# Kernel optimization log

Hardware: AMD Instinct MI355X
Metric: run time of the kernel (lower is better)

The kernel has to match this reference:

```python
import jax, jax.numpy as jnp
import numpy as np

WINDOW = 12
NUM_HEADS = 16

def window_partition(x, ws):
    b, h, w, c = x.shape
    x = x.reshape(b, h // ws, ws, w // ws, ws, c)
    return x.transpose(0, 1, 3, 2, 4, 5).reshape(-1, ws, ws, c)

def window_reverse(windows, ws, h, w):
    c = windows.shape[-1]
    x = windows.reshape(-1, h // ws, w // ws, ws, ws, c)
    return x.transpose(0, 1, 3, 2, 4, 5).reshape(-1, h, w, c)

def setup_inputs() -> dict:
    key = jax.random.key(0)
    ks = jax.random.split(key, 5)
    dim = 512
    hidden_states = jax.random.normal(ks[0], (8, 48, 48, dim), dtype=jnp.float32)
    qkv_w = jax.random.normal(ks[1], (dim, 3 * dim), dtype=jnp.float32) * 0.02
    qkv_b = jnp.zeros((3 * dim,), dtype=jnp.float32)
    proj_w = jax.random.normal(ks[2], (dim, dim), dtype=jnp.float32) * 0.02
    proj_b = jnp.zeros((dim,), dtype=jnp.float32)
    return {"hidden_states": hidden_states, "qkv_w": qkv_w, "qkv_b": qkv_b,
            "proj_w": proj_w, "proj_b": proj_b}

def reference(hidden_states, qkv_w, qkv_b, proj_w, proj_b):
    b, h, w, c = hidden_states.shape
    ws = WINDOW
    nh = NUM_HEADS
    hd = c // nh
    scale = hd ** -0.5
    pad_r = (ws - w % ws) % ws
    pad_b = (ws - h % ws) % ws
    x = jnp.pad(hidden_states, ((0, 0), (0, pad_b), (0, pad_r), (0, 0)))
    ph, pw = x.shape[1], x.shape[2]
    # [nW, ws*ws, C]
    xw = window_partition(x, ws).reshape(-1, ws * ws, c)
    nw, nt, _ = xw.shape
    qkv = (xw @ qkv_w + qkv_b).reshape(nw, nt, 3, nh, hd)
    qkv = qkv.transpose(2, 0, 3, 1, 4)  # [3, nW, nh, nt, hd]
    q, k, v = qkv[0], qkv[1], qkv[2]
    scores = jnp.einsum('wnqd,wnkd->wnqk', q, k) * scale
    attn = jax.nn.softmax(scores, axis=-1)
    out = jnp.einsum('wnqk,wnkd->wnqd', attn, v)  # [nW, nh, nt, hd]
    out = out.transpose(0, 2, 1, 3).reshape(nw, nt, c)
    out = out @ proj_w + proj_b
    out = out.reshape(-1, ws, ws, c)
    out = window_reverse(out, ws, ph, pw)
    out = out[:, :h, :w, :]
    return out.reshape(b, h * w, c)
```

## Files before the change

kernel.cpp:

```cpp
#include <hip/hip_runtime.h>
#include <hip/hip_bf16.h>


typedef unsigned short u16;
typedef unsigned int u32;
typedef __attribute__((ext_vector_type(4))) float f32x4;
typedef __attribute__((ext_vector_type(8))) short short8;

#define MFMA16(a, b, c) __builtin_amdgcn_mfma_f32_16x16x32_bf16(a, b, c, 0, 0, 0)
#define AS1 __attribute__((address_space(1)))
#define AS3 __attribute__((address_space(3)))

__device__ __forceinline__ u16 f2b(float f) {
  __hip_bfloat16 h = __float2bfloat16(f);
  return *reinterpret_cast<u16*>(&h);
}

__global__ void prep_x_kernel(const float* __restrict__ x, u16* __restrict__ xw) {
  int c = blockIdx.x * 256 + threadIdx.x;
  int r = c >> 6;
  int colb = (c & 63) << 3;
  int win = r / 144, tok = r - win * 144;
  int b = win >> 4, wh = (win >> 2) & 3, ww = win & 3;
  int i = tok / 12, j = tok - i * 12;
  const float* src = x + ((size_t)((b * 48 + wh * 12 + i) * 48 + ww * 12 + j)) * 512 + colb;
  float4 a0 = *(const float4*)(src);
  float4 a1 = *(const float4*)(src + 4);
  short8 o;
  o[0] = (short)f2b(a0.x); o[1] = (short)f2b(a0.y); o[2] = (short)f2b(a0.z); o[3] = (short)f2b(a0.w);
  o[4] = (short)f2b(a1.x); o[5] = (short)f2b(a1.y); o[6] = (short)f2b(a1.z); o[7] = (short)f2b(a1.w);
  *reinterpret_cast<short8*>(xw + (size_t)r * 512 + colb) = o;
}

__global__ void prep_wt_kernel(const float* __restrict__ w, u16* __restrict__ wt,
                               int K, int N) {
  int t = blockIdx.x * 256 + threadIdx.x;
  int nchunks = N >> 3;
  if (t >= K * nchunks) return;
  int k = t / nchunks;
  int n0 = (t - k * nchunks) << 3;
  const float* src = w + (size_t)k * N + n0;
  float4 a0 = *(const float4*)(src);
  float4 a1 = *(const float4*)(src + 4);
  float v[8] = {a0.x, a0.y, a0.z, a0.w, a1.x, a1.y, a1.z, a1.w};
#pragma unroll
  for (int j = 0; j < 8; j++) wt[(size_t)(n0 + j) * K + k] = f2b(v[j]);
}

template <int BM, int BN, int WM, int WN, int EPI>
__device__ __forceinline__ void gemm_impl(
    const u16* __restrict__ A, const u16* __restrict__ BT,
    const float* __restrict__ bias,
    u16* __restrict__ outb, float* __restrict__ outf,
    int M, int N, int K) {
  constexpr int MF = BM / WM / 16;
  constexpr int NF = BN / WN / 16;
  constexpr int ASLOT = BM * 32;
  constexpr int BSLOT = BN * 32;
  __shared__ __align__(16) u16 sA[4 * ASLOT];
  __shared__ __align__(16) u16 sB[4 * BSLOT];

  const int tid = threadIdx.x;
  const int wave = tid >> 6;
  const int lane = tid & 63;
  const int wm = wave / WN;
  const int wn = wave % WN;
  const int l15 = lane & 15;
  const int lhi = lane >> 4;

  const int nwg = gridDim.x;
  const int cpx = nwg >> 3;
  const int bid = (blockIdx.x & 7) * cpx + (blockIdx.x >> 3);
  const int nbn = N / BN;
  const int bn = bid % nbn;
  const int bm = bid / nbn;

  f32x4 acc[MF][NF];
  const f32x4 fzero = {0.f, 0.f, 0.f, 0.f};
#pragma unroll
  for (int i = 0; i < MF; i++)
#pragma unroll
    for (int j = 0; j < NF; j++) acc[i][j] = fzero;

  const int srow = lane >> 2;
  const int scol = (((lane & 3) ^ ((lane >> 3) & 3)) << 3);
  const int rcol = ((lhi ^ ((l15 >> 1) & 3)) << 3);

  const u16* Ab = A + (size_t)(bm * BM) * K;
  const u16* Bb = BT + (size_t)(bn * BN) * K;
  const int nt = K >> 5;

  auto stage = [&](int l, int tt) {
    const int slot = tt & 3;
    const int kk = tt << 5;
    if (l < 2) {
      const int c = wave * 2 + l;
      __builtin_amdgcn_global_load_lds(
          (const AS1 u32*)(Ab + (size_t)(c * 16 + srow) * K + kk + scol),
          (AS3 u32*)(&sA[slot * ASLOT + c * 512]), 16, 0, 0);
    } else {
      const int c = wave * 2 + (l - 2);
      __builtin_amdgcn_global_load_lds(
          (const AS1 u32*)(Bb + (size_t)(c * 16 + srow) * K + kk + scol),
          (AS3 u32*)(&sB[slot * BSLOT + c * 512]), 16, 0, 0);
    }
  };

#pragma unroll
  for (int t0 = 0; t0 < 3; ++t0)
#pragma unroll
    for (int l = 0; l < 4; ++l) stage(l, t0);

  for (int t = 0; t < nt; ++t) {
    const int cur = t & 3;
    const bool has3 = (t + 3 < nt);
    const int rem = nt - 1 - t;

    if (rem >= 2)      { asm volatile("s_waitcnt vmcnt(8)"); }
    else if (rem == 1) { asm volatile("s_waitcnt vmcnt(4)"); }
    else               { asm volatile("s_waitcnt vmcnt(0)"); }
    __builtin_amdgcn_sched_barrier(0);
    __builtin_amdgcn_s_barrier();
    __builtin_amdgcn_sched_barrier(0);

    const u16* pA = &sA[cur * ASLOT];
    const u16* pB = &sB[cur * BSLOT];

    short8 af[MF], bfr[NF];
#pragma unroll
    for (int m = 0; m < MF; ++m)
      af[m] = *reinterpret_cast<const short8*>(
          pA + (wm * (MF * 16) + m * 16 + l15) * 32 + rcol);
#pragma unroll
    for (int n = 0; n < NF; ++n)
      bfr[n] = *reinterpret_cast<const short8*>(
          pB + (wn * (NF * 16) + n * 16 + l15) * 32 + rcol);
    __builtin_amdgcn_sched_barrier(0);

    if (has3) {
#pragma unroll
      for (int l = 0; l < 4; ++l) stage(l, t + 3);
    }
    __builtin_amdgcn_sched_barrier(0);

    __builtin_amdgcn_s_setprio(1);
#pragma unroll
    for (int m = 0; m < MF; ++m)
#pragma unroll
      for (int n = 0; n < NF; ++n)
        acc[m][n] = MFMA16(af[m], bfr[n], acc[m][n]);
    __builtin_amdgcn_s_setprio(0);

    __builtin_amdgcn_sched_barrier(0);
    __builtin_amdgcn_s_barrier();
  }

#pragma unroll
  for (int i = 0; i < MF; ++i) {
    const int row0 = bm * BM + wm * (MF * 16) + i * 16 + lhi * 4;
#pragma unroll
    for (int j = 0; j < NF; ++j) {
      const int col = bn * BN + wn * (NF * 16) + j * 16 + l15;
      const float bv = bias[col];
#pragma unroll
      for (int r = 0; r < 4; ++r) {
        float v = acc[i][j][r] + bv;
        const int row = row0 + r;
        if (EPI == 0) {
          outb[(size_t)row * N + col] = f2b(v);
        } else {
          int win = row / 144, tok = row - win * 144;
          int b = win >> 4, wh = (win >> 2) & 3, ww = win & 3;
          int ii = tok / 12, jj = tok - ii * 12;
          size_t o = ((size_t)b * 2304 + (wh * 12 + ii) * 48 + (ww * 12 + jj)) * 512 + col;
          outf[o] = v;
        }
      }
    }
  }
}

__global__ __launch_bounds__(512, 1) void qkv_gemm(
    const u16* __restrict__ A, const u16* __restrict__ BT,
    const float* __restrict__ bias, u16* __restrict__ outb,
    int M, int N, int K) {
  gemm_impl<256, 256, 2, 4, 0>(A, BT, bias, outb, nullptr, M, N, K);
}

__global__ __launch_bounds__(256, 2) void proj_gemm(
    const u16* __restrict__ A, const u16* __restrict__ BT,
    const float* __restrict__ bias, float* __restrict__ outf,
    int M, int N, int K) {
  gemm_impl<128, 128, 2, 2, 1>(A, BT, bias, nullptr, outf, M, N, K);
}

__global__ __launch_bounds__(192) void attn_kernel(const u16* __restrict__ qkv,
                                                   u16* __restrict__ outb) {
  constexpr int PSTR = 168;
  __shared__ __align__(16) u16 sVT[32 * PSTR];
  __shared__ __align__(16) u16 sP[3 * 16 * PSTR];
  const int tid = threadIdx.x;
  const int wave = tid >> 6;
  const int lane = tid & 63;
  const int l15 = lane & 15;
  const int lhi = lane >> 4;
  const int win = blockIdx.x;
  const int head = blockIdx.y;
  const size_t base = ((size_t)win * 144) * 1536 + head * 32;
  const u16* Q = qkv + base;
  const u16* Kp = qkv + base + 512;
  const u16* V = qkv + base + 1024;
  constexpr float SC2 = 0.25509915922608635f;
  const f32x4 fzero = {0.f, 0.f, 0.f, 0.f};

  short8 vv[3];
  int vtok[3], vdb[3];
#pragma unroll
  for (int it = 0; it < 3; ++it) {
    int t = tid + it * 192;
    vtok[it] = t >> 2; vdb[it] = t & 3;
    vv[it] = *reinterpret_cast<const short8*>(V + (size_t)vtok[it] * 1536 + vdb[it] * 8);
  }
  short8 qa[3];
#pragma unroll
  for (int mt = 0; mt < 3; mt++) {
    int row = wave * 48 + mt * 16 + l15;
    qa[mt] = *reinterpret_cast<const short8*>(Q + (size_t)row * 1536 + lhi * 8);
  }
  short8 kb[9];
#pragma unroll
  for (int nt = 0; nt < 9; nt++) {
    int ctok = nt * 16 + l15;
    kb[nt] = *reinterpret_cast<const short8*>(Kp + (size_t)ctok * 1536 + lhi * 8);
  }

#pragma unroll
  for (int it = 0; it < 3; ++it) {
#pragma unroll
    for (int j = 0; j < 8; j++) sVT[(vdb[it] * 8 + j) * PSTR + vtok[it]] = (u16)vv[it][j];
  }
  for (int t = tid; t < 512; t += 192) {
    int d = t >> 4, cc = 144 + (t & 15);
    sVT[d * PSTR + cc] = 0;
  }
  u16* sPw = sP + wave * 16 * PSTR;
  for (int t = lane; t < 256; t += 64) {
    int rr = t >> 4, cc = 144 + (t & 15);
    sPw[rr * PSTR + cc] = 0;
  }

  __syncthreads();

  f32x4 o[3][2];
#pragma unroll
  for (int mt = 0; mt < 3; mt++)
#pragma unroll
    for (int nt = 0; nt < 2; nt++) o[mt][nt] = fzero;

#pragma unroll
  for (int mt = 0; mt < 3; mt++) {
    f32x4 s[9];
#pragma unroll
    for (int nt = 0; nt < 9; nt++) s[nt] = MFMA16(qa[mt], kb[nt], fzero);

#pragma unroll
    for (int r = 0; r < 4; r++) {
      float p[9], sum = 0.f;
#pragma unroll
      for (int nt = 0; nt < 9; nt++) {
        p[nt] = exp2f(s[nt][r] * SC2);
        sum += p[nt];
      }
#pragma unroll
      for (int off = 1; off < 16; off <<= 1) sum += __shfl_xor(sum, off, 64);
      float inv = 1.f / sum;
      int prow = lhi * 4 + r;
#pragma unroll
      for (int nt = 0; nt < 9; nt++)
        sPw[prow * PSTR + nt * 16 + l15] = f2b(p[nt] * inv);
    }

#pragma unroll
    for (int kk = 0; kk < 5; kk++) {
      short8 pa = *reinterpret_cast<const short8*>(sPw + l15 * PSTR + kk * 32 + lhi * 8);
#pragma unroll
      for (int nt = 0; nt < 2; nt++) {
        short8 vb = *reinterpret_cast<const short8*>(sVT + (nt * 16 + l15) * PSTR + kk * 32 + lhi * 8);
        o[mt][nt] = MFMA16(pa, vb, o[mt][nt]);
      }
    }
  }

  const int rowb = win * 144 + wave * 48;
#pragma unroll
  for (int mt = 0; mt < 3; mt++) {
#pragma unroll
    for (int nt = 0; nt < 2; nt++) {
      int col = head * 32 + nt * 16 + l15;
#pragma unroll
      for (int r = 0; r < 4; r++) {
        int row = rowb + mt * 16 + lhi * 4 + r;
        outb[(size_t)row * 512 + col] = f2b(o[mt][nt][r]);
      }
    }
  }
}

extern "C" void kernel_launch(void* const* d_in, const int* in_sizes, int n_in,
                              void* d_out, int out_size, void* d_ws, size_t ws_size,
                              hipStream_t stream) {
  const float* x      = (const float*)d_in[0];
  const float* qkv_w  = (const float*)d_in[1];
  const float* qkv_b  = (const float*)d_in[2];
  const float* proj_w = (const float*)d_in[3];
  const float* proj_b = (const float*)d_in[4];
  float* out = (float*)d_out;

  u16* xw     = (u16*)d_ws;
  u16* qkvT   = xw + (size_t)18432 * 512;
  u16* projT  = qkvT + (size_t)1536 * 512;
  u16* qkvout = projT + (size_t)512 * 512;
  u16* attno  = qkvout + (size_t)18432 * 1536;

  prep_x_kernel<<<4608, 256, 0, stream>>>(x, xw);
  prep_wt_kernel<<<384, 256, 0, stream>>>(qkv_w, qkvT, 512, 1536);
  prep_wt_kernel<<<128, 256, 0, stream>>>(proj_w, projT, 512, 512);

  qkv_gemm<<<432, 512, 0, stream>>>(xw, qkvT, qkv_b, qkvout, 18432, 1536, 512);

  attn_kernel<<<dim3(128, 16), 192, 0, stream>>>(qkvout, attno);

  proj_gemm<<<576, 256, 0, stream>>>(attno, projT, proj_b, out, 18432, 512, 512);
}
```

Measured before the change: 191.4 us.

## Write QKV in per-window-head layout with pre-transposed V; retile GEMMs

The QKV GEMM epilogue now scatters Q and K into contiguous per-(window,head) blocks and writes V already transposed with a padded stride. The attention kernel can then load V straight into LDS with global_load_lds, and its Q/K loads become contiguous. A new kernel clears the V padding columns. The GEMM pipeline drops from four LDS stages to two with a single barrier per step, and the QKV GEMM moves to 128x128 tiles with more blocks and higher occupancy. In exchange, the QKV epilogue stores become scattered 2-byte writes, and the shallower pipeline exposes more load latency.

```diff
diff --git a/kernel.cpp b/kernel.cpp
--- a/kernel.cpp
+++ b/kernel.cpp
@@ -10,6 +10,10 @@
 #define MFMA16(a, b, c) __builtin_amdgcn_mfma_f32_16x16x32_bf16(a, b, c, 0, 0, 0)
 #define AS1 __attribute__((address_space(1)))
 #define AS3 __attribute__((address_space(3)))
+
+constexpr size_t QTOT = (size_t)2048 * 4608;
+constexpr int VSTR = 176;
+constexpr size_t VWH = 32 * VSTR;
 
 __device__ __forceinline__ u16 f2b(float f) {
   __hip_bfloat16 h = __float2bfloat16(f);
@@ -47,6 +51,14 @@
   for (int j = 0; j < 8; j++) wt[(size_t)(n0 + j) * K + k] = f2b(v[j]);
 }
 
+__global__ void pad_clear_kernel(u16* __restrict__ vs) {
+  int wh = blockIdx.x;
+  int t = threadIdx.x;
+  int d = t >> 2, c = 144 + (t & 3) * 8;
+  short8 z = {0, 0, 0, 0, 0, 0, 0, 0};
+  *reinterpret_cast<short8*>(vs + (size_t)wh * VWH + d * VSTR + c) = z;
+}
+
 template <int BM, int BN, int WM, int WN, int EPI>
 __device__ __forceinline__ void gemm_impl(
     const u16* __restrict__ A, const u16* __restrict__ BT,
@@ -57,8 +69,8 @@
   constexpr int NF = BN / WN / 16;
   constexpr int ASLOT = BM * 32;
   constexpr int BSLOT = BN * 32;
-  __shared__ __align__(16) u16 sA[4 * ASLOT];
-  __shared__ __align__(16) u16 sB[4 * BSLOT];
+  __shared__ __align__(16) u16 sA[2 * ASLOT];
+  __shared__ __align__(16) u16 sB[2 * BSLOT];
 
   const int tid = threadIdx.x;
   const int wave = tid >> 6;
@@ -91,7 +103,7 @@
   const int nt = K >> 5;
 
   auto stage = [&](int l, int tt) {
-    const int slot = tt & 3;
+    const int slot = tt & 1;
     const int kk = tt << 5;
     if (l < 2) {
       const int c = wave * 2 + l;
@@ -107,18 +119,12 @@
   };
 
 #pragma unroll
-  for (int t0 = 0; t0 < 3; ++t0)
-#pragma unroll
-    for (int l = 0; l < 4; ++l) stage(l, t0);
+  for (int l = 0; l < 4; ++l) stage(l, 0);
 
   for (int t = 0; t < nt; ++t) {
-    const int cur = t & 3;
-    const bool has3 = (t + 3 < nt);
-    const int rem = nt - 1 - t;
-
-    if (rem >= 2)      { asm volatile("s_waitcnt vmcnt(8)"); }
-    else if (rem == 1) { asm volatile("s_waitcnt vmcnt(4)"); }
-    else               { asm volatile("s_waitcnt vmcnt(0)"); }
+    const int cur = t & 1;
+
+    asm volatile("s_waitcnt vmcnt(0)");
     __builtin_amdgcn_sched_barrier(0);
     __builtin_amdgcn_s_barrier();
     __builtin_amdgcn_sched_barrier(0);
@@ -137,9 +143,9 @@
           pB + (wn * (NF * 16) + n * 16 + l15) * 32 + rcol);
     __builtin_amdgcn_sched_barrier(0);
 
-    if (has3) {
-#pragma unroll
-      for (int l = 0; l < 4; ++l) stage(l, t + 3);
+    if (t + 1 < nt) {
+#pragma unroll
+      for (int l = 0; l < 4; ++l) stage(l, t + 1);
     }
     __builtin_amdgcn_sched_barrier(0);
 
@@ -150,9 +156,6 @@
       for (int n = 0; n < NF; ++n)
         acc[m][n] = MFMA16(af[m], bfr[n], acc[m][n]);
     __builtin_amdgcn_s_setprio(0);
-
-    __builtin_amdgcn_sched_barrier(0);
-    __builtin_amdgcn_s_barrier();
   }
 
 #pragma unroll
@@ -168,87 +171,94 @@
         const int row = row0 + r;
         if (EPI == 0) {
           outb[(size_t)row * N + col] = f2b(v);
-        } else {
+        } else if (EPI == 1) {
           int win = row / 144, tok = row - win * 144;
           int b = win >> 4, wh = (win >> 2) & 3, ww = win & 3;
           int ii = tok / 12, jj = tok - ii * 12;
           size_t o = ((size_t)b * 2304 + (wh * 12 + ii) * 48 + (ww * 12 + jj)) * 512 + col;
           outf[o] = v;
+        } else {
+          int dg = col & 511;
+          int typ = col >> 9;
+          int head = dg >> 5, d = dg & 31;
+          int win = row / 144, tok = row - win * 144;
+          int wh = win * 16 + head;
+          u16 bv16 = f2b(v);
+          if (typ == 0)
+            outb[(size_t)wh * 4608 + tok * 32 + d] = bv16;
+          else if (typ == 1)
+            outb[QTOT + (size_t)wh * 4608 + tok * 32 + d] = bv16;
+          else
+            outb[2 * QTOT + (size_t)wh * VWH + d * VSTR + tok] = bv16;
         }
       }
     }
   }
 }
 
-__global__ __launch_bounds__(512, 1) void qkv_gemm(
+__global__ __launch_bounds__(256, 4) void qkv_gemm(
     const u16* __restrict__ A, const u16* __restrict__ BT,
     const float* __restrict__ bias, u16* __restrict__ outb,
     int M, int N, int K) {
-  gemm_impl<256, 256, 2, 4, 0>(A, BT, bias, outb, nullptr, M, N, K);
-}
-
-__global__ __launch_bounds__(256, 2) void proj_gemm(
+  gemm_impl<128, 128, 2, 2, 2>(A, BT, bias, outb, nullptr, M, N, K);
+}
+
+__global__ __launch_bounds__(256, 4) void proj_gemm(
     const u16* __restrict__ A, const u16* __restrict__ BT,
     const float* __restrict__ bias, float* __restrict__ outf,
     int M, int N, int K) {
   gemm_impl<128, 128, 2, 2, 1>(A, BT, bias, nullptr, outf, M, N, K);
 }
 
-__global__ __launch_bounds__(192) void attn_kernel(const u16* __restrict__ qkv,
+__global__ __launch_bounds__(192) void attn_kernel(const u16* __restrict__ qkvs,
                                                    u16* __restrict__ outb) {
   constexpr int PSTR = 168;
-  __shared__ __align__(16) u16 sVT[32 * PSTR];
+  __shared__ __align__(16) u16 sVT[32 * VSTR];
   __shared__ __align__(16) u16 sP[3 * 16 * PSTR];
   const int tid = threadIdx.x;
   const int wave = tid >> 6;
   const int lane = tid & 63;
   const int l15 = lane & 15;
   const int lhi = lane >> 4;
-  const int win = blockIdx.x;
-  const int head = blockIdx.y;
-  const size_t base = ((size_t)win * 144) * 1536 + head * 32;
-  const u16* Q = qkv + base;
-  const u16* Kp = qkv + base + 512;
-  const u16* V = qkv + base + 1024;
+  const int wh = blockIdx.x;
+  const int win = wh >> 4;
+  const int head = wh & 15;
+  const u16* Q = qkvs + (size_t)wh * 4608;
+  const u16* Kp = qkvs + QTOT + (size_t)wh * 4608;
+  const u16* V = qkvs + 2 * QTOT + (size_t)wh * VWH;
   constexpr float SC2 = 0.25509915922608635f;
   const f32x4 fzero = {0.f, 0.f, 0.f, 0.f};
 
-  short8 vv[3];
-  int vtok[3], vdb[3];
-#pragma unroll
-  for (int it = 0; it < 3; ++it) {
-    int t = tid + it * 192;
-    vtok[it] = t >> 2; vdb[it] = t & 3;
-    vv[it] = *reinterpret_cast<const short8*>(V + (size_t)vtok[it] * 1536 + vdb[it] * 8);
-  }
+#pragma unroll
+  for (int i = 0; i < 4; ++i) {
+    const int c = wave * 4 + i;
+    if (c < 11) {
+      __builtin_amdgcn_global_load_lds(
+          (const AS1 u32*)(V + c * 512 + lane * 8),
+          (AS3 u32*)(&sVT[c * 512]), 16, 0, 0);
+    }
+  }
+
   short8 qa[3];
 #pragma unroll
   for (int mt = 0; mt < 3; mt++) {
     int row = wave * 48 + mt * 16 + l15;
-    qa[mt] = *reinterpret_cast<const short8*>(Q + (size_t)row * 1536 + lhi * 8);
+    qa[mt] = *reinterpret_cast<const short8*>(Q + row * 32 + lhi * 8);
   }
   short8 kb[9];
 #pragma unroll
   for (int nt = 0; nt < 9; nt++) {
     int ctok = nt * 16 + l15;
-    kb[nt] = *reinterpret_cast<const short8*>(Kp + (size_t)ctok * 1536 + lhi * 8);
-  }
-
-#pragma unroll
-  for (int it = 0; it < 3; ++it) {
-#pragma unroll
-    for (int j = 0; j < 8; j++) sVT[(vdb[it] * 8 + j) * PSTR + vtok[it]] = (u16)vv[it][j];
-  }
-  for (int t = tid; t < 512; t += 192) {
-    int d = t >> 4, cc = 144 + (t & 15);
-    sVT[d * PSTR + cc] = 0;
-  }
+    kb[nt] = *reinterpret_cast<const short8*>(Kp + ctok * 32 + lhi * 8);
+  }
+
   u16* sPw = sP + wave * 16 * PSTR;
   for (int t = lane; t < 256; t += 64) {
     int rr = t >> 4, cc = 144 + (t & 15);
     sPw[rr * PSTR + cc] = 0;
   }
 
+  asm volatile("s_waitcnt vmcnt(0)");
   __syncthreads();
 
   f32x4 o[3][2];
@@ -285,7 +295,7 @@
       short8 pa = *reinterpret_cast<const short8*>(sPw + l15 * PSTR + kk * 32 + lhi * 8);
 #pragma unroll
       for (int nt = 0; nt < 2; nt++) {
-        short8 vb = *reinterpret_cast<const short8*>(sVT + (nt * 16 + l15) * PSTR + kk * 32 + lhi * 8);
+        short8 vb = *reinterpret_cast<const short8*>(sVT + (nt * 16 + l15) * VSTR + kk * 32 + lhi * 8);
         o[mt][nt] = MFMA16(pa, vb, o[mt][nt]);
       }
     }
@@ -319,16 +329,17 @@
   u16* xw     = (u16*)d_ws;
   u16* qkvT   = xw + (size_t)18432 * 512;
   u16* projT  = qkvT + (size_t)1536 * 512;
-  u16* qkvout = projT + (size_t)512 * 512;
-  u16* attno  = qkvout + (size_t)18432 * 1536;
+  u16* qkvs   = projT + (size_t)512 * 512;
+  u16* attno  = qkvs + 2 * QTOT + (size_t)2048 * VWH;
 
   prep_x_kernel<<<4608, 256, 0, stream>>>(x, xw);
   prep_wt_kernel<<<384, 256, 0, stream>>>(qkv_w, qkvT, 512, 1536);
   prep_wt_kernel<<<128, 256, 0, stream>>>(proj_w, projT, 512, 512);
-
-  qkv_gemm<<<432, 512, 0, stream>>>(xw, qkvT, qkv_b, qkvout, 18432, 1536, 512);
-
-  attn_kernel<<<dim3(128, 16), 192, 0, stream>>>(qkvout, attno);
+  pad_clear_kernel<<<2048, 128, 0, stream>>>(qkvs + 2 * QTOT);
+
+  qkv_gemm<<<1728, 256, 0, stream>>>(xw, qkvT, qkv_b, qkvs, 18432, 1536, 512);
+
+  attn_kernel<<<2048, 192, 0, stream>>>(qkvs, attno);
 
   proj_gemm<<<576, 256, 0, stream>>>(attno, projT, proj_b, out, 18432, 512, 512);
 }
```

Result: slower. 217.4 us (+13.6%).
